# Kernel optimization log

Measured on AMD Instinct MI355X. Metric: run time of the kernel, lower is better.

## Reference

```python
import jax, jax.numpy as jnp
import numpy as np

B = 32768          # number of graphs
NN = 19            # nodes per graph
N = B * NN         # total nodes
EF_PER, ES_PER = 120, 60
NUM_BANDS = 5
EPS = 1e-5


def _make_edges(e_per, seed):
    r = np.random.default_rng(seed)
    s = r.integers(0, NN, e_per)
    d = r.integers(0, NN, e_per)
    off = (np.arange(B, dtype=np.int64) * NN)[:, None]
    src = (off + s[None, :]).reshape(-1).astype(np.int32)
    dst = (off + d[None, :]).reshape(-1).astype(np.int32)
    return np.stack([src, dst], axis=0)  # [2, B*e_per]


def setup_inputs() -> dict:
    key = jax.random.key(0)
    ks = jax.random.split(key, 16)
    inp = {
        "x": jax.random.normal(ks[0], (N, NUM_BANDS), jnp.float32),
        "edge_weight_func": jax.random.uniform(ks[1], (B * EF_PER,), jnp.float32),
        "edge_index_func": jnp.asarray(_make_edges(EF_PER, 1)),
        "edge_index_struct": jnp.asarray(_make_edges(ES_PER, 2)),
        # GCN band params
        "W1": jax.random.normal(ks[2], (NUM_BANDS, 1, 32), jnp.float32) * 0.5,
        "b1": jnp.zeros((NUM_BANDS, 32), jnp.float32),
        "g1": jnp.ones((NUM_BANDS, 32), jnp.float32),
        "bt1": jnp.zeros((NUM_BANDS, 32), jnp.float32),
        "W2": jax.random.normal(ks[3], (NUM_BANDS, 32, 2), jnp.float32) * 0.2,
        "b2": jnp.zeros((NUM_BANDS, 2), jnp.float32),
        "g2": jnp.ones((NUM_BANDS, 2), jnp.float32),
        "bt2": jnp.zeros((NUM_BANDS, 2), jnp.float32),
        # MLP head (kaiming-ish fan_in init)
        "lin1_W": jax.random.normal(ks[4], (190, 128), jnp.float32) * np.sqrt(2.0 / 190),
        "lin1_b": jnp.zeros((128,), jnp.float32),
        "g3": jnp.ones((128,), jnp.float32),
        "bt3": jnp.zeros((128,), jnp.float32),
        "lin2_W": jax.random.normal(ks[5], (128, 32), jnp.float32) * np.sqrt(2.0 / 128),
        "lin2_b": jnp.zeros((32,), jnp.float32),
        "lin3_W": jax.random.normal(ks[6], (32, 2), jnp.float32) * np.sqrt(2.0 / 32),
        "lin3_b": jnp.zeros((2,), jnp.float32),
    }
    return inp


def _bn(h, g, b):
    # BatchNorm1d with batch statistics (training-mode math, deterministic)
    m = h.mean(0)
    v = h.var(0)
    return (h - m) * jax.lax.rsqrt(v + EPS) * g + b


def _gcn(h_in, W, b, src, dst, ew, n):
    # PyG GCNConv: symmetric norm with self-loops (fill 1), linear then scatter-add
    h = h_in @ W                                   # [N, out]
    deg = jax.ops.segment_sum(ew, dst, num_segments=n) + 1.0  # self-loop weight 1
    dinv = jax.lax.rsqrt(deg)
    norm = dinv[src] * ew * dinv[dst]              # [E]
    agg = jax.ops.segment_sum(norm[:, None] * h[src], dst, num_segments=n)
    return agg + (dinv * dinv)[:, None] * h + b    # self-loop term + bias


def reference(x, edge_weight_func, W1, b1, g1, bt1, W2, b2, g2, bt2,
              lin1_W, lin1_b, g3, bt3, lin2_W, lin2_b, lin3_W, lin3_b,
              edge_index_func, edge_index_struct):
    n = x.shape[0]
    bsz = n // NN
    sf, df = edge_index_func[0], edge_index_func[1]
    ss, ds = edge_index_struct[0], edge_index_struct[1]
    ew_s = jnp.ones((ss.shape[0],), x.dtype)
    outs = []
    for i in range(NUM_BANDS):
        h = _gcn(x[:, i:i + 1], W1[i], b1[i], sf, df, edge_weight_func, n)
        h = jax.nn.relu(_bn(h, g1[i], bt1[i]))
        h = _gcn(h, W2[i], b2[i], ss, ds, ew_s, n)
        h = jax.nn.relu(_bn(h, g2[i], bt2[i]))
        outs.append(h.reshape(bsz, NN * 2))
    xc = jnp.concatenate(outs, axis=1)             # [B, 190]
    h = jax.nn.relu(_bn(xc @ lin1_W + lin1_b, g3, bt3))
    h = jax.nn.relu(h @ lin2_W + lin2_b)
    return h @ lin3_W + lin3_b                     # [B, 2]
```

## Files before the change

kernel.cpp:

```cpp
#include <hip/hip_runtime.h>

#define BGR 32768
#define NNODE 19
#define NTOT (BGR*NNODE)
#define EF 120
#define ES 60
#define NB 5
#define EPS 1e-5f

#define WS_U     0
#define WS_PRE2  (WS_U + NTOT*NB)
#define WS_PRE3  (WS_PRE2 + BGR*190)
#define WS_P3    (WS_PRE3 + BGR*128)
#define WS_R3    (WS_P3 + 262144)
#define WS_P1    (WS_R3 + 16384)
#define WS_R2    (WS_P1 + 1600)
#define WS_WP    (WS_R2 + 6400)
#define WS_TB    (WS_WP + 24576)
#define WS_TSEG  (WS_TB + 168)
#define WS_END   (WS_TSEG + 660)

__global__ __launch_bounds__(256) void k1_gcn1(
    const float* __restrict__ x, const float* __restrict__ ew,
    const int* __restrict__ srcf, const int* __restrict__ dstf,
    float* __restrict__ U)
{
    __shared__ float xg[4][96];
    __shared__ float Nr[4][400];
    __shared__ float dinv[4][20];
    int t = threadIdx.x, q = t >> 6, lane = t & 63;
    int g = blockIdx.x*4 + q;

    int s0, d0, s1 = 0, d1 = 0; float w0, w1 = 0.f;
    bool e1 = (lane < EF - 64);
    s0 = srcf[g*EF+lane] - g*NNODE; d0 = dstf[g*EF+lane] - g*NNODE; w0 = ew[g*EF+lane];
    if (e1) { s1 = srcf[g*EF+lane+64] - g*NNODE; d1 = dstf[g*EF+lane+64] - g*NNODE; w1 = ew[g*EF+lane+64]; }
    for (int i = lane; i < 95; i += 64) xg[q][i] = x[g*95 + i];
    for (int i = lane; i < 400; i += 64) Nr[q][i] = 0.f;
    __syncthreads();

    atomicAdd(&Nr[q][d0*21 + s0], w0);
    if (e1) atomicAdd(&Nr[q][d1*21 + s1], w1);
    __syncthreads();

    if (lane < NNODE) {
        float s = 0.f;
        #pragma unroll
        for (int k = 0; k < 19; k++) s += Nr[q][lane*21 + k];
        dinv[q][lane] = rsqrtf(s + 1.f);
    }
    __syncthreads();
    for (int i = lane; i < 95; i += 64) xg[q][i] *= dinv[q][i/5];
    __syncthreads();

    for (int i = lane; i < 95; i += 64) {
        int v = i/5, b = i - 5*v;
        float acc = xg[q][i];
        #pragma unroll
        for (int s = 0; s < 19; s++) acc += Nr[q][v*21 + s] * xg[q][s*5 + b];
        U[(size_t)g*95 + i] = dinv[q][v] * acc;
    }
}

__global__ __launch_bounds__(256) void kr1(const float* __restrict__ U, float* __restrict__ P1,
    const float* __restrict__ W, float* __restrict__ Wp)
{
    int t = threadIdx.x;
    if (blockIdx.x < 96) {
        int idx = blockIdx.x*256 + t;
        int k = idx >> 7, f = idx & 127;
        float val = 0.f;
        if (k < 190) {
            int p = k >> 1, kk = k & 1;
            int v = p/5, b = p - 5*v;
            val = W[(b*38 + v*2 + kk)*128 + f];
        }
        Wp[idx] = val;
    }
    const int CH = NTOT*NB/160;
    size_t base = (size_t)blockIdx.x * CH;
    float s[5], qq[5];
    #pragma unroll
    for (int b = 0; b < 5; b++) { s[b] = 0.f; qq[b] = 0.f; }
    int m = (int)((base + t) % 5);
    for (int n = 0; n < CH/256; n++) {
        float v = U[base + n*256 + t];
        #pragma unroll
        for (int b = 0; b < 5; b++) {
            bool hit = (m == b);
            s[b]  += hit ? v   : 0.f;
            qq[b] += hit ? v*v : 0.f;
        }
        m++; if (m == 5) m = 0;
    }
    __shared__ float red[256][10];
    #pragma unroll
    for (int b = 0; b < 5; b++) { red[t][b] = s[b]; red[t][5+b] = qq[b]; }
    __syncthreads();
    for (int off = 128; off > 0; off >>= 1) {
        if (t < off) {
            #pragma unroll
            for (int k = 0; k < 10; k++) red[t][k] += red[t+off][k];
        }
        __syncthreads();
    }
    if (t < 10) P1[blockIdx.x*10 + t] = red[0][t];
}

__global__ __launch_bounds__(256) void k2c(const float* __restrict__ P1,
    const float* __restrict__ W1, const float* __restrict__ g1, const float* __restrict__ bt1,
    const float* __restrict__ W2, float* __restrict__ TB, float4* __restrict__ TSEG)
{
    __shared__ float red[16][10];
    __shared__ float mean[5], varr[5];
    __shared__ float4 T1s[160];
    __shared__ float  traw[5][32];
    __shared__ float4 dlt[5][32];
    __shared__ float  acc0[5][4];
    int t = threadIdx.x;

    if (t < 160) {
        int col = t % 10, grp = t / 10;
        float acc = 0.f;
        for (int j = 0; j < 10; j++) acc += P1[(grp*10 + j)*10 + col];
        red[grp][col] = acc;
    }
    if (t < 20) ((float*)acc0)[t] = 0.f;
    __syncthreads();
    if (t < 10) {
        float ss = 0.f;
        #pragma unroll
        for (int j = 0; j < 16; j++) ss += red[j][t];
        red[0][t] = ss;
    }
    __syncthreads();
    if (t < 5) {
        float m = red[0][t] / (float)NTOT;
        mean[t] = m;
        varr[t] = red[0][5+t] / (float)NTOT - m*m;
    }
    __syncthreads();

    int b = 0, f = 0; float a = 0.f, d = 0.f, wx = 0.f, wy = 0.f, tf = 0.f; bool dg = true;
    if (t < 160) {
        b = t >> 5; f = t & 31;
        float w = W1[t];
        a = w * rsqrtf(w*w*varr[b] + EPS) * g1[t];
        d = bt1[t] - a*mean[b];
        wx = W2[t*2]; wy = W2[t*2+1];
        dg = (fabsf(a) < 1e-30f);
        tf = dg ? 3.0e38f : (-d/a);
        traw[b][f] = tf;
        if (dg) {
            float rd = fmaxf(d, 0.f);
            atomicAdd(&acc0[b][1], wx*rd);
            atomicAdd(&acc0[b][3], wy*rd);
        } else if (a < 0.f) {
            atomicAdd(&acc0[b][0], wx*a);
            atomicAdd(&acc0[b][1], wx*d);
            atomicAdd(&acc0[b][2], wy*a);
            atomicAdd(&acc0[b][3], wy*d);
        }
    }
    __syncthreads();
    if (t < 160) {
        int r = 0;
        #pragma unroll
        for (int ff = 0; ff < 32; ff++) {
            float o = traw[b][ff];
            r += (o < tf || (o == tf && ff < f)) ? 1 : 0;
        }
        TB[b*33 + r] = tf;
        float4 dl = make_float4(0.f, 0.f, 0.f, 0.f);
        if (!dg) {
            float sgn = (a > 0.f) ? 1.f : -1.f;
            dl = make_float4(sgn*wx*a, sgn*wx*d, sgn*wy*a, sgn*wy*d);
        }
        dlt[b][r] = dl;
    }
    if (t < 5) TB[t*33 + 32] = 3.0e38f;
    __syncthreads();
    if (t < 5) {
        float sx = acc0[t][0], cx = acc0[t][1], sy = acc0[t][2], cy = acc0[t][3];
        TSEG[t*33 + 0] = make_float4(sx, cx, sy, cy);
        for (int r = 0; r < 32; r++) {
            float4 dl = dlt[t][r];
            sx += dl.x; cx += dl.y; sy += dl.z; cy += dl.w;
            TSEG[t*33 + r + 1] = make_float4(sx, cx, sy, cy);
        }
    }
    (void)T1s;
}

__global__ __launch_bounds__(256) void k3b(
    const float* __restrict__ U, const int* __restrict__ srcs, const int* __restrict__ dsts,
    const float* __restrict__ TBg, const float4* __restrict__ TSEGg,
    const float* __restrict__ b2, float2* __restrict__ pre2)
{
    __shared__ float  tt[168];
    __shared__ float4 tseg[165];
    __shared__ float2 h2l[4][96];
    __shared__ float  Mr[4][400];
    __shared__ float  dinv[4][20];
    __shared__ float  b2l[12];
    int t = threadIdx.x, q = t >> 6, lane = t & 63;
    int g = blockIdx.x*4 + q;

    if (t < 165) { tt[t] = TBg[t]; tseg[t] = TSEGg[t]; }
    float u0 = U[(size_t)g*95 + lane];
    float u1 = (lane < 31) ? U[(size_t)g*95 + lane + 64] : 0.f;
    int ls = 0, ld = 0; bool ee = (lane < ES);
    if (ee) { ls = srcs[g*ES+lane] - g*NNODE; ld = dsts[g*ES+lane] - g*NNODE; }
    if (t < 10) b2l[t] = b2[t];
    for (int i = lane; i < 400; i += 64) Mr[q][i] = 0.f;
    __syncthreads();

    if (ee) atomicAdd(&Mr[q][ld*21 + ls], 1.f);
    __syncthreads();

    if (lane < NNODE) {
        float s = 0.f;
        #pragma unroll
        for (int k = 0; k < 19; k++) s += Mr[q][lane*21 + k];
        dinv[q][lane] = rsqrtf(s + 1.f);
    }
    __syncthreads();

    {
        int v0 = lane/5, b0 = lane - 5*v0;
        int j = 0;
        #pragma unroll
        for (int st = 32; st > 0; st >>= 1) {
            int nx = j + st;
            if (nx <= 32 && u0 >= tt[b0*33 + nx - 1]) j = nx;
        }
        float4 sc = tseg[b0*33 + j];
        float dv = dinv[q][v0];
        h2l[q][lane] = make_float2(dv*fmaf(sc.x, u0, sc.y), dv*fmaf(sc.z, u0, sc.w));
        if (lane < 31) {
            int i1 = lane + 64, v1 = i1/5, b1 = i1 - 5*v1;
            int j1 = 0;
            #pragma unroll
            for (int st = 32; st > 0; st >>= 1) {
                int nx = j1 + st;
                if (nx <= 32 && u1 >= tt[b1*33 + nx - 1]) j1 = nx;
            }
            float4 sc1 = tseg[b1*33 + j1];
            float dv1 = dinv[q][v1];
            h2l[q][i1] = make_float2(dv1*fmaf(sc1.x, u1, sc1.y), dv1*fmaf(sc1.z, u1, sc1.w));
        }
    }
    __syncthreads();

    for (int i = lane; i < 95; i += 64) {
        int v = i/5, b = i - 5*v;
        float2 self = h2l[q][i];
        float ax = self.x, ay = self.y;
        #pragma unroll
        for (int s = 0; s < 19; s++) {
            float m = Mr[q][v*21 + s];
            float2 hh = h2l[q][s*5 + b];
            ax = fmaf(m, hh.x, ax);
            ay = fmaf(m, hh.y, ay);
        }
        float dv = dinv[q][v];
        pre2[(size_t)g*95 + i] = make_float2(fmaf(dv, ax, b2l[2*b]),
                                             fmaf(dv, ay, b2l[2*b+1]));
    }
}

__global__ __launch_bounds__(256) void kr2(const float2* __restrict__ pre2, float* __restrict__ r2)
{
    int t = threadIdx.x;
    size_t base = (size_t)blockIdx.x * 9728;
    float sx[5], sy[5], qx[5], qy[5];
    #pragma unroll
    for (int b = 0; b < 5; b++) { sx[b]=0.f; sy[b]=0.f; qx[b]=0.f; qy[b]=0.f; }
    for (int n = 0; n < 38; n++) {
        size_t i = base + n*256 + t;
        float2 v = pre2[i];
        int p = (int)(i % 95);
        int b = p % 5;
        #pragma unroll
        for (int bb = 0; bb < 5; bb++) {
            bool m = (b == bb);
            sx[bb] += m ? v.x : 0.f;     sy[bb] += m ? v.y : 0.f;
            qx[bb] += m ? v.x*v.x : 0.f; qy[bb] += m ? v.y*v.y : 0.f;
        }
    }
    __shared__ float red[256][20];
    #pragma unroll
    for (int b = 0; b < 5; b++) {
        red[t][2*b] = sx[b];      red[t][2*b+1] = sy[b];
        red[t][10+2*b] = qx[b];   red[t][11+2*b] = qy[b];
    }
    __syncthreads();
    for (int off = 128; off > 0; off >>= 1) {
        if (t < off) {
            #pragma unroll
            for (int k = 0; k < 20; k++) red[t][k] += red[t+off][k];
        }
        __syncthreads();
    }
    if (t < 20) r2[blockIdx.x*20 + t] = red[0][t];
}

__global__ __launch_bounds__(256, 4) void k5_lin1(
    const float2* __restrict__ pre2, const float* __restrict__ R2,
    const float* __restrict__ g2, const float* __restrict__ bt2,
    const float* __restrict__ Wp, const float* __restrict__ bias,
    float* __restrict__ pre3, float* __restrict__ p3)
{
    __shared__ float xg[32*192];
    __shared__ float a2l[10], d2l[10];
    __shared__ float r20[12][20];
    __shared__ float redS[8][128], redQ[8][128];
    int t = threadIdx.x, bid = blockIdx.x;

    if (t < 240) {
        int col = t % 20, grp = t / 20;
        float s = 0.f;
        for (int j = grp; j < 320; j += 12) s += R2[j*20 + col];
        r20[grp][col] = s;
    }
    if (t >= 240 && t < 240+16) {
        int i = t - 240;
    }
    __syncthreads();
    if (t < 20) {
        float s = 0.f;
        #pragma unroll
        for (int j = 0; j < 12; j++) s += r20[j][t];
        r20[0][t] = s;
    }
    if (t < 64) xg[(t>>1)*192 + 190 + (t&1)] = 0.f;
    __syncthreads();
    if (t < 10) {
        float m = r20[0][t] / (float)NTOT;
        float v = r20[0][10+t] / (float)NTOT - m*m;
        float a = g2[t] * rsqrtf(v + EPS);
        a2l[t] = a;
        d2l[t] = bt2[t] - a*m;
    }
    __syncthreads();

    const float2* src = pre2 + (size_t)bid*3040;
    for (int i = t; i < 3040; i += 256) {
        int gg = i / 95, p = i - gg*95;
        int b = p % 5;
        float2 v = src[i];
        xg[gg*192 + 2*p]     = fmaxf(fmaf(a2l[2*b],   v.x, d2l[2*b]),   0.f);
        xg[gg*192 + 2*p + 1] = fmaxf(fmaf(a2l[2*b+1], v.y, d2l[2*b+1]), 0.f);
    }
    __syncthreads();

    int lane = t & 63, h = t >> 6;
    int f32 = lane & 31, gh = lane >> 5;
    const float* xh = xg + (h*8 + gh*4)*192;
    float acc[4][4];
    #pragma unroll
    for (int r = 0; r < 4; r++)
        #pragma unroll
        for (int c = 0; c < 4; c++) acc[r][c] = 0.f;

    for (int kt = 0; kt < 24; kt++) {
        float4 w[8];
        #pragma unroll
        for (int j = 0; j < 8; j++)
            w[j] = *(const float4*)(Wp + (kt*8 + j)*128 + 4*f32);
        #pragma unroll
        for (int r = 0; r < 4; r++) {
            float4 xa = *(const float4*)(xh + r*192 + kt*8);
            float4 xb = *(const float4*)(xh + r*192 + kt*8 + 4);
            #pragma unroll
            for (int c = 0; c < 4; c++) {
                float a = acc[r][c];
                a = fmaf(xa.x, ((const float*)&w[0])[c], a);
                a = fmaf(xa.y, ((const float*)&w[1])[c], a);
                a = fmaf(xa.z, ((const float*)&w[2])[c], a);
                a = fmaf(xa.w, ((const float*)&w[3])[c], a);
                a = fmaf(xb.x, ((const float*)&w[4])[c], a);
                a = fmaf(xb.y, ((const float*)&w[5])[c], a);
                a = fmaf(xb.z, ((const float*)&w[6])[c], a);
                a = fmaf(xb.w, ((const float*)&w[7])[c], a);
                acc[r][c] = a;
            }
        }
    }

    int gbase = bid*32 + h*8 + gh*4;
    float4 b4 = *(const float4*)(bias + 4*f32);
    float s4[4] = {0.f,0.f,0.f,0.f}, q4[4] = {0.f,0.f,0.f,0.f};
    #pragma unroll
    for (int r = 0; r < 4; r++) {
        float4 pv;
        pv.x = acc[r][0] + b4.x;
        pv.y = acc[r][1] + b4.y;
        pv.z = acc[r][2] + b4.z;
        pv.w = acc[r][3] + b4.w;
        *(float4*)(pre3 + (size_t)(gbase + r)*128 + 4*f32) = pv;
        s4[0]+=pv.x; s4[1]+=pv.y; s4[2]+=pv.z; s4[3]+=pv.w;
        q4[0]+=pv.x*pv.x; q4[1]+=pv.y*pv.y; q4[2]+=pv.z*pv.z; q4[3]+=pv.w*pv.w;
    }
    *(float4*)&redS[h*2 + gh][4*f32] = make_float4(s4[0], s4[1], s4[2], s4[3]);
    *(float4*)&redQ[h*2 + gh][4*f32] = make_float4(q4[0], q4[1], q4[2], q4[3]);
    __syncthreads();
    if (t < 128) {
        float s = 0.f;
        #pragma unroll
        for (int j = 0; j < 8; j++) s += redS[j][t];
        p3[bid*256 + t] = s;
    } else {
        int f = t - 128;
        float qq = 0.f;
        #pragma unroll
        for (int j = 0; j < 8; j++) qq += redQ[j][f];
        p3[bid*256 + 128 + f] = qq;
    }
}

__global__ __launch_bounds__(256) void k6a(const float* __restrict__ p3, float* __restrict__ r3)
{
    int j = blockIdx.x, f = threadIdx.x;
    float s = 0.f;
    for (int r = j*16; r < (j+1)*16; r++) s += p3[r*256 + f];
    r3[j*256 + f] = s;
}

__global__ __launch_bounds__(256) void k7_head(
    const float* __restrict__ pre3, const float* __restrict__ R3,
    const float* __restrict__ g3, const float* __restrict__ bt3,
    const float* __restrict__ W2h, const float* __restrict__ b2h,
    const float* __restrict__ W3h, const float* __restrict__ b3h,
    float* __restrict__ out)
{
    __shared__ float A3s[128], D3s[128];
    int t = threadIdx.x;
    if (t < 128) {
        float s = 0.f, q = 0.f;
        for (int j = 0; j < 64; j++) { s += R3[j*256 + t]; q += R3[j*256 + 128 + t]; }
        float m = s / (float)BGR;
        float v = q / (float)BGR - m*m;
        float a = g3[t] * rsqrtf(v + EPS);
        A3s[t] = a;
        D3s[t] = bt3[t] - a*m;
    }
    __syncthreads();

    int g = blockIdx.x*256 + t;
    float accj[32];
    #pragma unroll
    for (int j = 0; j < 32; j++) accj[j] = b2h[j];
    const float* p3 = pre3 + (size_t)g*128;
    #pragma unroll 2
    for (int f4 = 0; f4 < 128; f4 += 4) {
        float4 pv = *(const float4*)(p3 + f4);
        float y0 = fmaxf(fmaf(A3s[f4+0], pv.x, D3s[f4+0]), 0.f);
        float y1 = fmaxf(fmaf(A3s[f4+1], pv.y, D3s[f4+1]), 0.f);
        float y2 = fmaxf(fmaf(A3s[f4+2], pv.z, D3s[f4+2]), 0.f);
        float y3 = fmaxf(fmaf(A3s[f4+3], pv.w, D3s[f4+3]), 0.f);
        #pragma unroll
        for (int j = 0; j < 32; j++) {
            accj[j] = fmaf(y0, W2h[(f4+0)*32+j], accj[j]);
            accj[j] = fmaf(y1, W2h[(f4+1)*32+j], accj[j]);
            accj[j] = fmaf(y2, W2h[(f4+2)*32+j], accj[j]);
            accj[j] = fmaf(y3, W2h[(f4+3)*32+j], accj[j]);
        }
    }
    float o0 = b3h[0], o1 = b3h[1];
    #pragma unroll
    for (int j = 0; j < 32; j++) {
        float yj = fmaxf(accj[j], 0.f);
        o0 = fmaf(yj, W3h[j*2+0], o0);
        o1 = fmaf(yj, W3h[j*2+1], o1);
    }
    ((float2*)out)[g] = make_float2(o0, o1);
}

extern "C" void kernel_launch(void* const* d_in, const int* in_sizes, int n_in,
                              void* d_out, int out_size, void* d_ws, size_t ws_size,
                              hipStream_t stream)
{
    (void)in_sizes; (void)n_in; (void)out_size; (void)ws_size;
    const float* x    = (const float*)d_in[0];
    const float* ew   = (const float*)d_in[1];
    const int*   eif  = (const int*)d_in[2];
    const int*   eis  = (const int*)d_in[3];
    const float* W1   = (const float*)d_in[4];
    const float* g1   = (const float*)d_in[6];
    const float* bt1  = (const float*)d_in[7];
    const float* W2   = (const float*)d_in[8];
    const float* b2   = (const float*)d_in[9];
    const float* g2   = (const float*)d_in[10];
    const float* bt2  = (const float*)d_in[11];
    const float* l1W  = (const float*)d_in[12];
    const float* l1b  = (const float*)d_in[13];
    const float* g3   = (const float*)d_in[14];
    const float* bt3  = (const float*)d_in[15];
    const float* l2W  = (const float*)d_in[16];
    const float* l2b  = (const float*)d_in[17];
    const float* l3W  = (const float*)d_in[18];
    const float* l3b  = (const float*)d_in[19];
    float* out = (float*)d_out;
    float* ws  = (float*)d_ws;

    const int* srcf = eif;  const int* dstf = eif + BGR*EF;
    const int* srcs = eis;  const int* dsts = eis + BGR*ES;

    float* U    = ws + WS_U;
    float* PRE2 = ws + WS_PRE2;
    float* PRE3 = ws + WS_PRE3;
    float* P3   = ws + WS_P3;
    float* R3   = ws + WS_R3;
    float* P1   = ws + WS_P1;
    float* R2   = ws + WS_R2;
    float* WP   = ws + WS_WP;
    float* TB   = ws + WS_TB;
    float4* TSEG= (float4*)(ws + WS_TSEG);

    k1_gcn1<<<BGR/4, 256, 0, stream>>>(x, ew, srcf, dstf, U);
    kr1<<<160, 256, 0, stream>>>(U, P1, l1W, WP);
    k2c<<<1, 256, 0, stream>>>(P1, W1, g1, bt1, W2, TB, TSEG);
    k3b<<<BGR/4, 256, 0, stream>>>(U, srcs, dsts, TB, TSEG, b2, (float2*)PRE2);
    kr2<<<320, 256, 0, stream>>>((const float2*)PRE2, R2);
    k5_lin1<<<1024, 256, 0, stream>>>((const float2*)PRE2, R2, g2, bt2, WP, l1b, PRE3, P3);
    k6a<<<64, 256, 0, stream>>>(P3, R3);
    k7_head<<<BGR/256, 256, 0, stream>>>(PRE3, R3, g3, bt3, l2W, l2b, l3W, l3b, out);
}
```

Baseline: 307.8 us.

## Retune grid sizes, vectorize per-graph aggregation, and split head MLP across lanes

Several changes land together. The per-graph adjacency matrices in both GCN kernels drop from a stride-21 to a stride-20 layout, and the node features become band-major and zero-padded, so the neighbour sums can use float4 shared-memory reads. The reduction kernels kr1 and kr2 get more blocks (640) with smaller chunks, and the k2c and k5 partial-sum readers are updated to match. k5_lin1 doubles its per-block tile to 64 graphs with 8 rows per thread and drops the occupancy hint. The head kernel splits each graph across two lanes and combines the halves with shuffles, which gives more parallel threads at the cost of extra shuffle work.

```diff
diff --git a/kernel.cpp b/kernel.cpp
--- a/kernel.cpp
+++ b/kernel.cpp
@@ -12,20 +12,19 @@
 #define WS_PRE2  (WS_U + NTOT*NB)
 #define WS_PRE3  (WS_PRE2 + BGR*190)
 #define WS_P3    (WS_PRE3 + BGR*128)
-#define WS_R3    (WS_P3 + 262144)
+#define WS_R3    (WS_P3 + 131072)
 #define WS_P1    (WS_R3 + 16384)
-#define WS_R2    (WS_P1 + 1600)
-#define WS_WP    (WS_R2 + 6400)
+#define WS_R2    (WS_P1 + 6400)
+#define WS_WP    (WS_R2 + 12800)
 #define WS_TB    (WS_WP + 24576)
 #define WS_TSEG  (WS_TB + 168)
-#define WS_END   (WS_TSEG + 660)
 
 __global__ __launch_bounds__(256) void k1_gcn1(
     const float* __restrict__ x, const float* __restrict__ ew,
     const int* __restrict__ srcf, const int* __restrict__ dstf,
     float* __restrict__ U)
 {
-    __shared__ float xg[4][96];
+    __shared__ float xgb[4][100];
     __shared__ float Nr[4][400];
     __shared__ float dinv[4][20];
     int t = threadIdx.x, q = t >> 6, lane = t & 63;
@@ -35,29 +34,41 @@
     bool e1 = (lane < EF - 64);
     s0 = srcf[g*EF+lane] - g*NNODE; d0 = dstf[g*EF+lane] - g*NNODE; w0 = ew[g*EF+lane];
     if (e1) { s1 = srcf[g*EF+lane+64] - g*NNODE; d1 = dstf[g*EF+lane+64] - g*NNODE; w1 = ew[g*EF+lane+64]; }
-    for (int i = lane; i < 95; i += 64) xg[q][i] = x[g*95 + i];
+    for (int j = lane; j < 100; j += 64) {
+        int b = j/20, s = j - 20*b;
+        xgb[q][j] = (s < 19) ? x[g*95 + s*5 + b] : 0.f;
+    }
     for (int i = lane; i < 400; i += 64) Nr[q][i] = 0.f;
     __syncthreads();
 
-    atomicAdd(&Nr[q][d0*21 + s0], w0);
-    if (e1) atomicAdd(&Nr[q][d1*21 + s1], w1);
-    __syncthreads();
-
-    if (lane < NNODE) {
-        float s = 0.f;
-        #pragma unroll
-        for (int k = 0; k < 19; k++) s += Nr[q][lane*21 + k];
-        dinv[q][lane] = rsqrtf(s + 1.f);
-    }
-    __syncthreads();
-    for (int i = lane; i < 95; i += 64) xg[q][i] *= dinv[q][i/5];
+    atomicAdd(&Nr[q][d0*20 + s0], w0);
+    if (e1) atomicAdd(&Nr[q][d1*20 + s1], w1);
+    __syncthreads();
+
+    if (lane < 20) {
+        float dv = 0.f;
+        if (lane < 19) {
+            float s = 0.f;
+            #pragma unroll
+            for (int k = 0; k < 19; k++) s += Nr[q][lane*20 + k];
+            dv = rsqrtf(s + 1.f);
+        }
+        dinv[q][lane] = dv;
+    }
+    __syncthreads();
+    for (int j = lane; j < 100; j += 64) xgb[q][j] *= dinv[q][j % 20];
     __syncthreads();
 
     for (int i = lane; i < 95; i += 64) {
         int v = i/5, b = i - 5*v;
-        float acc = xg[q][i];
-        #pragma unroll
-        for (int s = 0; s < 19; s++) acc += Nr[q][v*21 + s] * xg[q][s*5 + b];
+        float acc = xgb[q][b*20 + v];
+        const float4* nrp = (const float4*)&Nr[q][v*20];
+        const float4* xbp = (const float4*)&xgb[q][b*20];
+        #pragma unroll
+        for (int j = 0; j < 5; j++) {
+            float4 n4 = nrp[j], x4 = xbp[j];
+            acc += n4.x*x4.x + n4.y*x4.y + n4.z*x4.z + n4.w*x4.w;
+        }
         U[(size_t)g*95 + i] = dinv[q][v] * acc;
     }
 }
@@ -77,7 +88,7 @@
         }
         Wp[idx] = val;
     }
-    const int CH = NTOT*NB/160;
+    const int CH = NTOT*NB/640;
     size_t base = (size_t)blockIdx.x * CH;
     float s[5], qq[5];
     #pragma unroll
@@ -113,7 +124,6 @@
 {
     __shared__ float red[16][10];
     __shared__ float mean[5], varr[5];
-    __shared__ float4 T1s[160];
     __shared__ float  traw[5][32];
     __shared__ float4 dlt[5][32];
     __shared__ float  acc0[5][4];
@@ -122,7 +132,7 @@
     if (t < 160) {
         int col = t % 10, grp = t / 10;
         float acc = 0.f;
-        for (int j = 0; j < 10; j++) acc += P1[(grp*10 + j)*10 + col];
+        for (int j = grp; j < 640; j += 16) acc += P1[j*10 + col];
         red[grp][col] = acc;
     }
     if (t < 20) ((float*)acc0)[t] = 0.f;
@@ -189,7 +199,6 @@
             TSEG[t*33 + r + 1] = make_float4(sx, cx, sy, cy);
         }
     }
-    (void)T1s;
 }
 
 __global__ __launch_bounds__(256) void k3b(
@@ -199,7 +208,7 @@
 {
     __shared__ float  tt[168];
     __shared__ float4 tseg[165];
-    __shared__ float2 h2l[4][96];
+    __shared__ float2 h2b[4][100];
     __shared__ float  Mr[4][400];
     __shared__ float  dinv[4][20];
     __shared__ float  b2l[12];
@@ -215,14 +224,18 @@
     for (int i = lane; i < 400; i += 64) Mr[q][i] = 0.f;
     __syncthreads();
 
-    if (ee) atomicAdd(&Mr[q][ld*21 + ls], 1.f);
-    __syncthreads();
-
-    if (lane < NNODE) {
-        float s = 0.f;
-        #pragma unroll
-        for (int k = 0; k < 19; k++) s += Mr[q][lane*21 + k];
-        dinv[q][lane] = rsqrtf(s + 1.f);
+    if (ee) atomicAdd(&Mr[q][ld*20 + ls], 1.f);
+    __syncthreads();
+
+    if (lane < 20) {
+        float dv = 0.f;
+        if (lane < 19) {
+            float s = 0.f;
+            #pragma unroll
+            for (int k = 0; k < 19; k++) s += Mr[q][lane*20 + k];
+            dv = rsqrtf(s + 1.f);
+        }
+        dinv[q][lane] = dv;
     }
     __syncthreads();
 
@@ -236,7 +249,7 @@
         }
         float4 sc = tseg[b0*33 + j];
         float dv = dinv[q][v0];
-        h2l[q][lane] = make_float2(dv*fmaf(sc.x, u0, sc.y), dv*fmaf(sc.z, u0, sc.w));
+        h2b[q][b0*20 + v0] = make_float2(dv*fmaf(sc.x, u0, sc.y), dv*fmaf(sc.z, u0, sc.w));
         if (lane < 31) {
             int i1 = lane + 64, v1 = i1/5, b1 = i1 - 5*v1;
             int j1 = 0;
@@ -247,21 +260,24 @@
             }
             float4 sc1 = tseg[b1*33 + j1];
             float dv1 = dinv[q][v1];
-            h2l[q][i1] = make_float2(dv1*fmaf(sc1.x, u1, sc1.y), dv1*fmaf(sc1.z, u1, sc1.w));
-        }
+            h2b[q][b1*20 + v1] = make_float2(dv1*fmaf(sc1.x, u1, sc1.y), dv1*fmaf(sc1.z, u1, sc1.w));
+        }
+        if (lane < 5) h2b[q][lane*20 + 19] = make_float2(0.f, 0.f);
     }
     __syncthreads();
 
     for (int i = lane; i < 95; i += 64) {
         int v = i/5, b = i - 5*v;
-        float2 self = h2l[q][i];
+        float2 self = h2b[q][b*20 + v];
         float ax = self.x, ay = self.y;
-        #pragma unroll
-        for (int s = 0; s < 19; s++) {
-            float m = Mr[q][v*21 + s];
-            float2 hh = h2l[q][s*5 + b];
-            ax = fmaf(m, hh.x, ax);
-            ay = fmaf(m, hh.y, ay);
+        const float4* mp = (const float4*)&Mr[q][v*20];
+        const float4* hp = (const float4*)&h2b[q][b*20];
+        #pragma unroll
+        for (int j = 0; j < 5; j++) {
+            float4 m4 = mp[j];
+            float4 hA = hp[2*j], hB = hp[2*j+1];
+            ax += m4.x*hA.x + m4.y*hA.z + m4.z*hB.x + m4.w*hB.z;
+            ay += m4.x*hA.y + m4.y*hA.w + m4.z*hB.y + m4.w*hB.w;
         }
         float dv = dinv[q][v];
         pre2[(size_t)g*95 + i] = make_float2(fmaf(dv, ax, b2l[2*b]),
@@ -272,11 +288,11 @@
 __global__ __launch_bounds__(256) void kr2(const float2* __restrict__ pre2, float* __restrict__ r2)
 {
     int t = threadIdx.x;
-    size_t base = (size_t)blockIdx.x * 9728;
+    size_t base = (size_t)blockIdx.x * 4864;
     float sx[5], sy[5], qx[5], qy[5];
     #pragma unroll
     for (int b = 0; b < 5; b++) { sx[b]=0.f; sy[b]=0.f; qx[b]=0.f; qy[b]=0.f; }
-    for (int n = 0; n < 38; n++) {
+    for (int n = 0; n < 19; n++) {
         size_t i = base + n*256 + t;
         float2 v = pre2[i];
         int p = (int)(i % 95);
@@ -305,13 +321,13 @@
     if (t < 20) r2[blockIdx.x*20 + t] = red[0][t];
 }
 
-__global__ __launch_bounds__(256, 4) void k5_lin1(
+__global__ __launch_bounds__(256) void k5_lin1(
     const float2* __restrict__ pre2, const float* __restrict__ R2,
     const float* __restrict__ g2, const float* __restrict__ bt2,
     const float* __restrict__ Wp, const float* __restrict__ bias,
     float* __restrict__ pre3, float* __restrict__ p3)
 {
-    __shared__ float xg[32*192];
+    __shared__ float xg[64*192];
     __shared__ float a2l[10], d2l[10];
     __shared__ float r20[12][20];
     __shared__ float redS[8][128], redQ[8][128];
@@ -320,12 +336,10 @@
     if (t < 240) {
         int col = t % 20, grp = t / 20;
         float s = 0.f;
-        for (int j = grp; j < 320; j += 12) s += R2[j*20 + col];
+        for (int j = grp; j < 640; j += 12) s += R2[j*20 + col];
         r20[grp][col] = s;
     }
-    if (t >= 240 && t < 240+16) {
-        int i = t - 240;
-    }
+    if (t < 128) xg[(t >> 1)*192 + 190 + (t & 1)] = 0.f;
     __syncthreads();
     if (t < 20) {
         float s = 0.f;
@@ -333,7 +347,6 @@
         for (int j = 0; j < 12; j++) s += r20[j][t];
         r20[0][t] = s;
     }
-    if (t < 64) xg[(t>>1)*192 + 190 + (t&1)] = 0.f;
     __syncthreads();
     if (t < 10) {
         float m = r20[0][t] / (float)NTOT;
@@ -344,8 +357,8 @@
     }
     __syncthreads();
 
-    const float2* src = pre2 + (size_t)bid*3040;
-    for (int i = t; i < 3040; i += 256) {
+    const float2* src = pre2 + (size_t)bid*6080;
+    for (int i = t; i < 6080; i += 256) {
         int gg = i / 95, p = i - gg*95;
         int b = p % 5;
         float2 v = src[i];
@@ -356,10 +369,10 @@
 
     int lane = t & 63, h = t >> 6;
     int f32 = lane & 31, gh = lane >> 5;
-    const float* xh = xg + (h*8 + gh*4)*192;
-    float acc[4][4];
-    #pragma unroll
-    for (int r = 0; r < 4; r++)
+    const float* xh = xg + (h*16 + gh*8)*192;
+    float acc[8][4];
+    #pragma unroll
+    for (int r = 0; r < 8; r++)
         #pragma unroll
         for (int c = 0; c < 4; c++) acc[r][c] = 0.f;
 
@@ -369,7 +382,7 @@
         for (int j = 0; j < 8; j++)
             w[j] = *(const float4*)(Wp + (kt*8 + j)*128 + 4*f32);
         #pragma unroll
-        for (int r = 0; r < 4; r++) {
+        for (int r = 0; r < 8; r++) {
             float4 xa = *(const float4*)(xh + r*192 + kt*8);
             float4 xb = *(const float4*)(xh + r*192 + kt*8 + 4);
             #pragma unroll
@@ -388,11 +401,11 @@
         }
     }
 
-    int gbase = bid*32 + h*8 + gh*4;
+    int gbase = bid*64 + h*16 + gh*8;
     float4 b4 = *(const float4*)(bias + 4*f32);
     float s4[4] = {0.f,0.f,0.f,0.f}, q4[4] = {0.f,0.f,0.f,0.f};
     #pragma unroll
-    for (int r = 0; r < 4; r++) {
+    for (int r = 0; r < 8; r++) {
         float4 pv;
         pv.x = acc[r][0] + b4.x;
         pv.y = acc[r][1] + b4.y;
@@ -423,7 +436,7 @@
 {
     int j = blockIdx.x, f = threadIdx.x;
     float s = 0.f;
-    for (int r = j*16; r < (j+1)*16; r++) s += p3[r*256 + f];
+    for (int r = j*8; r < (j+1)*8; r++) s += p3[r*256 + f];
     r3[j*256 + f] = s;
 }
 
@@ -447,34 +460,44 @@
     }
     __syncthreads();
 
-    int g = blockIdx.x*256 + t;
+    int gi = t >> 1, half = t & 1;
+    int g = blockIdx.x*128 + gi;
+    const float* p3 = pre3 + (size_t)g*128 + half*64;
+    const float* A3h = A3s + half*64;
+    const float* D3h = D3s + half*64;
     float accj[32];
     #pragma unroll
-    for (int j = 0; j < 32; j++) accj[j] = b2h[j];
-    const float* p3 = pre3 + (size_t)g*128;
+    for (int j = 0; j < 32; j++) accj[j] = half ? 0.f : b2h[j];
     #pragma unroll 2
-    for (int f4 = 0; f4 < 128; f4 += 4) {
+    for (int f4 = 0; f4 < 64; f4 += 4) {
         float4 pv = *(const float4*)(p3 + f4);
-        float y0 = fmaxf(fmaf(A3s[f4+0], pv.x, D3s[f4+0]), 0.f);
-        float y1 = fmaxf(fmaf(A3s[f4+1], pv.y, D3s[f4+1]), 0.f);
-        float y2 = fmaxf(fmaf(A3s[f4+2], pv.z, D3s[f4+2]), 0.f);
-        float y3 = fmaxf(fmaf(A3s[f4+3], pv.w, D3s[f4+3]), 0.f);
+        float y0 = fmaxf(fmaf(A3h[f4+0], pv.x, D3h[f4+0]), 0.f);
+        float y1 = fmaxf(fmaf(A3h[f4+1], pv.y, D3h[f4+1]), 0.f);
+        float y2 = fmaxf(fmaf(A3h[f4+2], pv.z, D3h[f4+2]), 0.f);
+        float y3 = fmaxf(fmaf(A3h[f4+3], pv.w, D3h[f4+3]), 0.f);
+        const float* w = W2h + (half*64 + f4)*32;
         #pragma unroll
         for (int j = 0; j < 32; j++) {
-            accj[j] = fmaf(y0, W2h[(f4+0)*32+j], accj[j]);
-            accj[j] = fmaf(y1, W2h[(f4+1)*32+j], accj[j]);
-            accj[j] = fmaf(y2, W2h[(f4+2)*32+j], accj[j]);
-            accj[j] = fmaf(y3, W2h[(f4+3)*32+j], accj[j]);
-        }
-    }
-    float o0 = b3h[0], o1 = b3h[1];
-    #pragma unroll
-    for (int j = 0; j < 32; j++) {
-        float yj = fmaxf(accj[j], 0.f);
-        o0 = fmaf(yj, W3h[j*2+0], o0);
-        o1 = fmaf(yj, W3h[j*2+1], o1);
-    }
-    ((float2*)out)[g] = make_float2(o0, o1);
+            accj[j] = fmaf(y0, w[j],      accj[j]);
+            accj[j] = fmaf(y1, w[32+j],   accj[j]);
+            accj[j] = fmaf(y2, w[64+j],   accj[j]);
+            accj[j] = fmaf(y3, w[96+j],   accj[j]);
+        }
+    }
+    #pragma unroll
+    for (int j = 0; j < 32; j++) accj[j] += __shfl_xor(accj[j], 1);
+    float o0 = half ? 0.f : b3h[0];
+    float o1 = half ? 0.f : b3h[1];
+    int j0 = half*16;
+    #pragma unroll
+    for (int j = 0; j < 16; j++) {
+        float yj = fmaxf(accj[j0 + j], 0.f);
+        o0 = fmaf(yj, W3h[(j0+j)*2+0], o0);
+        o1 = fmaf(yj, W3h[(j0+j)*2+1], o1);
+    }
+    o0 += __shfl_xor(o0, 1);
+    o1 += __shfl_xor(o1, 1);
+    if (!half) ((float2*)out)[g] = make_float2(o0, o1);
 }
 
 extern "C" void kernel_launch(void* const* d_in, const int* in_sizes, int n_in,
@@ -519,11 +542,11 @@
     float4* TSEG= (float4*)(ws + WS_TSEG);
 
     k1_gcn1<<<BGR/4, 256, 0, stream>>>(x, ew, srcf, dstf, U);
-    kr1<<<160, 256, 0, stream>>>(U, P1, l1W, WP);
+    kr1<<<640, 256, 0, stream>>>(U, P1, l1W, WP);
     k2c<<<1, 256, 0, stream>>>(P1, W1, g1, bt1, W2, TB, TSEG);
     k3b<<<BGR/4, 256, 0, stream>>>(U, srcs, dsts, TB, TSEG, b2, (float2*)PRE2);
-    kr2<<<320, 256, 0, stream>>>((const float2*)PRE2, R2);
-    k5_lin1<<<1024, 256, 0, stream>>>((const float2*)PRE2, R2, g2, bt2, WP, l1b, PRE3, P3);
+    kr2<<<640, 256, 0, stream>>>((const float2*)PRE2, R2);
+    k5_lin1<<<512, 256, 0, stream>>>((const float2*)PRE2, R2, g2, bt2, WP, l1b, PRE3, P3);
     k6a<<<64, 256, 0, stream>>>(P3, R3);
-    k7_head<<<BGR/256, 256, 0, stream>>>(PRE3, R3, g3, bt3, l2W, l2b, l3W, l3b, out);
-}
+    k7_head<<<256, 256, 0, stream>>>(PRE3, R3, g3, bt3, l2W, l2b, l3W, l3b, out);
+}
```

Result: no change. 310.1 us (+0.7%).
